# Kernel optimization log

Hardware: AMD Instinct MI355X
Metric: run time of the kernel (lower is better)

The kernel has to match this reference:

```python
import jax, jax.numpy as jnp
import numpy as np
from jax import lax


def ternarize(w):
    """Standard TWN ternarization with straight-through estimator.
    delta = 0.7*mean(|w|); alpha = mean(|w|) over kept entries; w_t = alpha*sign(w)*mask.
    """
    a = jnp.abs(w)
    delta = 0.7 * a.mean()
    mask = (a > delta).astype(w.dtype)
    alpha = (a * mask).sum() / jnp.maximum(mask.sum(), 1.0)
    wt = alpha * jnp.sign(w) * mask
    return w + lax.stop_gradient(wt - w)  # STE


def conv3x3(x, w, b):
    y = lax.conv_general_dilated(x, ternarize(w), window_strides=(1, 1),
                                 padding=((1, 1), (1, 1)),
                                 dimension_numbers=('NCHW', 'OIHW', 'NCHW'))
    return y + b[None, :, None, None]


def maxpool2(x):
    return lax.reduce_window(x, -jnp.inf, lax.max, (1, 1, 2, 2), (1, 1, 2, 2), 'VALID')


def setup_inputs() -> dict:
    key = jax.random.key(0)
    ks = jax.random.split(key, 11)
    s = lambda k, shape, scale: jax.random.normal(k, shape, dtype=jnp.float32) * scale
    return {
        'x':   s(ks[0], (1024, 3, 32, 32), 1.0),
        'w1':  s(ks[1], (64, 3, 3, 3), 0.1),
        'b1':  s(ks[2], (64,), 0.01),
        'w2':  s(ks[3], (128, 64, 3, 3), 0.05),
        'b2':  s(ks[4], (128,), 0.01),
        'w3':  s(ks[5], (256, 128, 3, 3), 0.03),
        'b3':  s(ks[6], (256,), 0.01),
        'wf1': s(ks[7], (256, 4096), 0.02),
        'bf1': s(ks[8], (256,), 0.01),
        'wf2': s(ks[9], (10, 256), 0.06),
        'bf2': s(ks[10], (10,), 0.01),
    }


def reference(x, w1, b1, w2, b2, w3, b3, wf1, bf1, wf2, bf2):
    x = maxpool2(jax.nn.relu(conv3x3(x, w1, b1)))   # [B,64,16,16]
    x = maxpool2(jax.nn.relu(conv3x3(x, w2, b2)))   # [B,128,8,8]
    x = maxpool2(jax.nn.relu(conv3x3(x, w3, b3)))   # [B,256,4,4]
    x = x.reshape(-1, 256 * 4 * 4)
    x = jax.nn.relu(x @ ternarize(wf1).T + bf1)     # [B,256]
    return x @ ternarize(wf2).T + bf2               # [B,10]
```

## Files before the change

### kernel.cpp

```cpp
#include <hip/hip_runtime.h>
#include <hip/hip_bf16.h>


typedef __attribute__((ext_vector_type(8))) short short8;
typedef __attribute__((ext_vector_type(4))) float f32x4;
typedef __attribute__((ext_vector_type(4))) int i32x4;

#define GLOAD_LDS16(g, l)                                              \
    __builtin_amdgcn_global_load_lds(                                  \
        (const __attribute__((address_space(1))) void*)(g),            \
        (__attribute__((address_space(3))) void*)(l), 16, 0, 0)

__device__ __forceinline__ unsigned short f2bf(float x) {
    unsigned u = __float_as_uint(x);
    return (unsigned short)((u + 0x7fffu + ((u >> 16) & 1u)) >> 16);
}
__device__ __forceinline__ float bf2f(unsigned short b) {
    return __uint_as_float(((unsigned)b) << 16);
}

__device__ __forceinline__ float calc_S1(const double* __restrict__ scr,
                                         float amaxx) {
    const double c2 = scr[2];
    const float alpha1 = (float)(scr[1] / (c2 > 1.0 ? c2 : 1.0));
    const float ub = alpha1 * (float)scr[22] * amaxx + (float)scr[23];
    return 32512.0f / fmaxf(ub, 1e-30f);
}
__device__ __forceinline__ float calc_S2(const double* __restrict__ scr,
                                         float amax1) {
    const double c2 = scr[6];
    const float alpha2 = (float)(scr[5] / (c2 > 1.0 ? c2 : 1.0));
    const float ub = alpha2 * (float)scr[24] * amax1 + (float)scr[25];
    return 32512.0f / fmaxf(ub, 1e-30f);
}

#define WS_W1B   0
#define N_W1B    2048
#define WS_W2P   (WS_W1B + N_W1B)
#define N_W2P    (9*128*64)
#define WS_W3P   (WS_W2P + N_W2P)
#define N_W3P    (9*256*128)
#define WS_WTF1  (WS_W3P + N_W3P)
#define N_WTF1   (256*4096)
#define WS_WTF2  (WS_WTF1 + N_WTF1)
#define N_WTF2   (10*256)
#define WS_A1    (WS_WTF2 + N_WTF2)
#define N_A1     (1024*256*64)
#define WS_A2    (WS_A1 + N_A1)
#define N_A2     (1024*64*128)
#define WS_A3    (WS_A2 + N_A2)
#define N_A3     (1024*16*256)
#define WS_F1    (WS_A3 + N_A3)
#define N_F1     (1024*256)
#define WS_SCR   (WS_F1 + N_F1)

#define FC1_S    16

struct TernArgs {
    const float* w[6];
    int n[6];
};

__global__ void tern_stats1(TernArgs ta, double* __restrict__ scr) {
    const int wi = blockIdx.y;
    const float* __restrict__ w = ta.w[wi];
    const int n = ta.n[wi];
    __shared__ double red[4];
    const int lane = threadIdx.x & 63, wv = threadIdx.x >> 6;
    if (wi == 5) {
        float m = 0.f;
        for (int i = blockIdx.x * blockDim.x + threadIdx.x; i < n;
             i += gridDim.x * blockDim.x)
            m = fmaxf(m, fabsf(w[i]));
        #pragma unroll
        for (int off = 32; off > 0; off >>= 1)
            m = fmaxf(m, __shfl_down(m, off, 64));
        if (lane == 0) red[wv] = (double)m;
        __syncthreads();
        if (threadIdx.x == 0) {
            float mm = (float)fmax(fmax(red[0], red[1]), fmax(red[2], red[3]));
            atomicMax((int*)(scr + 20), __float_as_int(mm));
        }
        return;
    }
    double s = 0.0;
    for (int i = blockIdx.x * blockDim.x + threadIdx.x; i < n;
         i += gridDim.x * blockDim.x)
        s += (double)fabsf(w[i]);
    #pragma unroll
    for (int off = 32; off > 0; off >>= 1) s += __shfl_down(s, off, 64);
    if (lane == 0) red[wv] = s;
    __syncthreads();
    if (threadIdx.x == 0)
        atomicAdd(scr + wi * 4, red[0] + red[1] + red[2] + red[3]);
}

__global__ void tern_stats2(TernArgs ta, double* __restrict__ scr) {
    const int wi = blockIdx.y;
    const float* __restrict__ w = ta.w[wi];
    const int n = ta.n[wi];
    const float delta = (float)(0.7 * scr[wi * 4] / (double)n);
    double ms = 0.0, cnt = 0.0;
    for (int i = blockIdx.x * blockDim.x + threadIdx.x; i < n;
         i += gridDim.x * blockDim.x) {
        float a = fabsf(w[i]);
        if (a > delta) { ms += (double)a; cnt += 1.0; }
    }
    #pragma unroll
    for (int off = 32; off > 0; off >>= 1) {
        ms += __shfl_down(ms, off, 64);
        cnt += __shfl_down(cnt, off, 64);
    }
    __shared__ double redm[4], redc[4];
    const int lane = threadIdx.x & 63, wv = threadIdx.x >> 6;
    if (lane == 0) { redm[wv] = ms; redc[wv] = cnt; }
    __syncthreads();
    if (threadIdx.x == 0) {
        atomicAdd(scr + wi * 4 + 1, redm[0] + redm[1] + redm[2] + redm[3]);
        atomicAdd(scr + wi * 4 + 2, redc[0] + redc[1] + redc[2] + redc[3]);
    }
}

__global__ void nnz_pass(const float* __restrict__ w1,
                         const float* __restrict__ b1,
                         const float* __restrict__ w2,
                         const float* __restrict__ b2,
                         double* __restrict__ scr) {
    __shared__ int sc1[2], sc2[2];
    __shared__ float sb1[2], sb2[2];
    const int t = threadIdx.x;
    const int lane = t & 63, wv = t >> 6;

    const float d1 = (float)(0.7 * scr[0] / 1728.0);
    int c1 = 0; float bb1 = 0.f;
    if (t < 64) {
        #pragma unroll
        for (int k = 0; k < 27; k++)
            c1 += (fabsf(w1[t * 27 + k]) > d1) ? 1 : 0;
        bb1 = fabsf(b1[t]);
    }
    const float d2 = (float)(0.7 * scr[4] / 73728.0);
    int c2 = 0;
    for (int k = 0; k < 576; k++)
        c2 += (fabsf(w2[t * 576 + k]) > d2) ? 1 : 0;
    float bb2 = fabsf(b2[t]);

    #pragma unroll
    for (int off = 32; off > 0; off >>= 1) {
        c1 = max(c1, __shfl_down(c1, off, 64));
        c2 = max(c2, __shfl_down(c2, off, 64));
        bb1 = fmaxf(bb1, __shfl_down(bb1, off, 64));
        bb2 = fmaxf(bb2, __shfl_down(bb2, off, 64));
    }
    if (lane == 0) { sc1[wv] = c1; sc2[wv] = c2; sb1[wv] = bb1; sb2[wv] = bb2; }
    __syncthreads();
    if (t == 0) {
        scr[22] = (double)max(sc1[0], sc1[1]);
        scr[23] = (double)fmaxf(sb1[0], sb1[1]);
        scr[24] = (double)max(sc2[0], sc2[1]);
        scr[25] = (double)fmaxf(sb2[0], sb2[1]);
    }
}

__global__ void tern_write_all(TernArgs ta, const double* __restrict__ scr,
                               signed char* __restrict__ w1b,
                               signed char* __restrict__ w2p8,
                               signed char* __restrict__ w3p8,
                               unsigned short* __restrict__ wtf1b,
                               float* __restrict__ wtf2) {
    const int wi = blockIdx.y;
    const float* __restrict__ w = ta.w[wi];
    const int n = ta.n[wi];
    const double* sc = scr + wi * 4;
    const float delta = (float)(0.7 * sc[0] / (double)n);
    const int i0 = blockIdx.x * blockDim.x + threadIdx.x;
    const int stride = gridDim.x * blockDim.x;

    if (wi == 0) {
        for (int i = i0; i < n; i += stride) {
            const int co = i / 27;
            const int kp = i % 27;
            float v = w[i];
            signed char s = (fabsf(v) > delta) ? (v > 0.0f ? 1 : -1) : 0;
            w1b[co * 64 + kp] = s;
            w1b[4096 + co * 64 + 32 + kp] = s;
        }
    } else if (wi == 4) {
        const double c = sc[2];
        const float alpha = (float)(sc[1] / (c > 1.0 ? c : 1.0));
        for (int i = i0; i < n; i += stride) {
            float v = w[i];
            wtf2[i] = (fabsf(v) > delta) ? (v > 0.0f ? alpha : -alpha) : 0.0f;
        }
    } else if (wi == 1 || wi == 2) {
        const int CIc = (wi == 1) ? 64 : 128;
        const int COc = (wi == 1) ? 128 : 256;
        signed char* dst = (wi == 1) ? w2p8 : w3p8;
        for (int i = i0; i < n; i += stride) {
            const int co = i / (CIc * 9);
            const int r = i % (CIc * 9);
            const int ci = r / 9, tap = r % 9;
            float v = w[i];
            signed char s = (fabsf(v) > delta) ? (v > 0.0f ? 1 : -1) : 0;
            dst[(tap * COc + co) * CIc + ci] = s;
        }
    } else {
        for (int i = i0; i < n; i += stride) {
            const int j = i >> 12;
            const int k = i & 4095;
            const int c = k >> 4, px = k & 15;
            float v = w[i];
            unsigned short s = (fabsf(v) > delta) ? (v > 0.0f ? 0x3f80 : 0xbf80) : 0;
            unsigned short* row = wtf1b + ((long)j << 13) + px * 512 + c;
            row[0] = s;
            row[256] = s;
        }
    }
}

__global__ __launch_bounds__(256) void conv1_i8(
        const float* __restrict__ x,
        const signed char* __restrict__ w1b,
        const float* __restrict__ bias,
        const double* __restrict__ scr,
        const int* __restrict__ amax_x,
        int* __restrict__ amax_out,
        signed char* __restrict__ a1q) {
    constexpr int PL = 3472;
    __shared__ __align__(16) char X[2 * PL];
    __shared__ float redm[4];

    const int b = blockIdx.x;
    const int tid = threadIdx.x;
    const float amx = fmaxf(__int_as_float(*amax_x), 1e-30f);
    const float S = 32512.0f / amx;
    const float S1 = calc_S1(scr, __int_as_float(*amax_x));

    for (int i = tid; i < 2 * PL / 16; i += 256)
        ((int4*)X)[i] = make_int4(0, 0, 0, 0);
    __syncthreads();

    for (int i = tid; i < 768; i += 256) {
        const float4 v = ((const float4*)(x + (long)b * 3072))[i];
        const int e = i * 4;
        const int ci = e >> 10;
        const int rem = e & 1023;
        const int h = rem >> 5, w = rem & 31;
        const int base = ci * 1156 + (h + 1) * 34 + (w + 1);
        const float f[4] = {v.x, v.y, v.z, v.w};
        #pragma unroll
        for (int j = 0; j < 4; j++) {
            const int q = __float2int_rn(f[j] * S);
            const int ql = (q << 24) >> 24;
            const int qh = (q - ql) >> 8;
            X[base + j] = (char)ql;
            X[PL + base + j] = (char)qh;
        }
    }
    __syncthreads();

    const int lane = tid & 63;
    const int wid = tid >> 6;
    const int lm = lane & 15;
    const int kg = lane >> 4;

    const int poff = (kg >= 2) ? PL : 0;
    int cst[16];
    #pragma unroll
    for (int j = 0; j < 16; j++) {
        const int kp = (kg & 1) * 16 + j;
        cst[j] = (kp < 27)
                     ? ((kp / 9) * 1156 + ((kp % 9) / 3) * 34 + (kp % 9) % 3)
                     : 0;
    }

    i32x4 BL[4], BH[4];
    #pragma unroll
    for (int nt = 0; nt < 4; nt++) {
        const int co = nt * 16 + lm;
        BL[nt] = *(const i32x4*)(w1b + (long)co * 64 + kg * 16);
        BH[nt] = *(const i32x4*)(w1b + 4096 + (long)co * 64 + kg * 16);
    }

    const double c2 = scr[2];
    const float alpha = (float)(scr[1] / (c2 > 1.0 ? c2 : 1.0));
    const float dq = alpha / S;
    float tmax = 0.f;
    signed char* yb = a1q + (long)b * 32768;

    for (int tt = 0; tt < 16; ++tt) {
        const int t = wid * 16 + tt;
        const int pp = t * 4 + (lm >> 2);
        const int sub = lm & 3;
        const int h = 2 * (pp >> 4) + (sub >> 1);
        const int w = 2 * (pp & 15) + (sub & 1);
        const int base = poff + h * 34 + w;
        unsigned d[4] = {0u, 0u, 0u, 0u};
        #pragma unroll
        for (int j = 0; j < 16; j++) {
            const unsigned byte = (unsigned char)X[base + cst[j]];
            d[j >> 2] |= byte << ((j & 3) * 8);
        }
        i32x4 Af;
        Af[0] = (int)d[0]; Af[1] = (int)d[1];
        Af[2] = (int)d[2]; Af[3] = (int)d[3];

        const int opp = t * 4 + kg;
        const int ho = opp >> 4, wo = opp & 15;
        signed char* yrow = yb + ((long)ho * 2048) + wo * 64;
        #pragma unroll
        for (int nt = 0; nt < 4; nt++) {
            i32x4 aL = 0, aH = 0;
            aL = __builtin_amdgcn_mfma_i32_16x16x64_i8(Af, BL[nt], aL, 0, 0, 0);
            aH = __builtin_amdgcn_mfma_i32_16x16x64_i8(Af, BH[nt], aH, 0, 0, 0);
            const int s0 = aH[0] * 256 + aL[0];
            const int s1 = aH[1] * 256 + aL[1];
            const int s2 = aH[2] * 256 + aL[2];
            const int s3 = aH[3] * 256 + aL[3];
            int sm = s0 > s1 ? s0 : s1;
            const int sn = s2 > s3 ? s2 : s3;
            sm = sm > sn ? sm : sn;
            const int co = nt * 16 + lm;
            const float o = fmaxf(dq * (float)sm + bias[co], 0.f);
            tmax = fmaxf(tmax, o);
            const int q = (int)(o * S1 + 0.5f);
            const int ql = (q << 24) >> 24;
            const int qh = (q + 128) >> 8;
            const int slot = (nt + ((wo + 1) >> 1) + 2 * (ho + 1)) & 3;
            const int off = slot * 16 + lm;
            yrow[off] = (char)ql;
            yrow[1024 + off] = (char)qh;
        }
    }

    #pragma unroll
    for (int off = 32; off > 0; off >>= 1)
        tmax = fmaxf(tmax, __shfl_down(tmax, off, 64));
    if (lane == 0) redm[wid] = tmax;
    __syncthreads();
    if (tid == 0) {
        float m = fmaxf(fmaxf(redm[0], redm[1]), fmaxf(redm[2], redm[3]));
        atomicMax(amax_out, __float_as_int(m));
    }
}

template <int CI, int HI, int CO, int HB, int WM, int WN, int MODE, int WIDX>
__global__ __launch_bounds__(256, 2) void conv_i8(
        const signed char* __restrict__ xin,
        const signed char* __restrict__ wp,
        const float* __restrict__ bias,
        const double* __restrict__ scr,
        const int* __restrict__ amax_x,
        const int* __restrict__ amax_1,
        void* __restrict__ yout) {
    constexpr int CH8 = CI / 64;
    constexpr int NITER = 9 * CH8;
    constexpr int HR = HI / HB;
    constexpr int ROWS = HR + 2;
    constexpr int COLS = HI + 2;
    constexpr int NPIX = ROWS * COLS;
    constexpr int PSTR = NPIX * 64 + 32;
    constexpr int PO = HI / 2;
    constexpr int POR = HR / 2;
    constexpr int MT = 4, NT = 4;
    constexpr int NPL = 2 * CH8;
    constexpr int RWQ = HI * 64 * 2;
    static_assert(WM * WN == 4, "4 waves");
    static_assert(WM * 64 == HR * HI, "M covers slab pixels");
    static_assert(WN * 64 == CO, "N covers all co");
    static_assert(MODE != 0 || (CI == 64 && RWQ == 2048), "conv2 shape");
    static_assert(MODE != 1 || (CI == 128 && HB == 1), "conv3 shape");
    static_assert(HB <= 2, "row compaction assumes <=1 invalid row per end");
    static_assert((COLS & 1) == 0, "swizzle parity uses even COLS");

    __shared__ __align__(16) char X[NPL * PSTR];
    __shared__ __align__(16) char RAW2[(MODE == 1) ? 16384 : 16];

    const int bimg = blockIdx.x / HB;
    const int hb = blockIdx.x % HB;
    const int tid = threadIdx.x;
    const int lane = tid & 63;
    const int wid = tid >> 6;

    const float S_in = (MODE == 0)
                           ? calc_S1(scr, __int_as_float(*amax_x))
                           : calc_S2(scr, __int_as_float(*amax_1));

    const int rlo = (hb == 0) ? 1 : 0;
    const int rhi = (hb == HB - 1) ? (ROWS - 1) : ROWS;

    if (MODE == 0) {
        for (int r = rlo; r < rhi; r++) {
            #pragma unroll
            for (int pl = 0; pl < 2; pl++) {
                if (wid == ((r * 2 + pl) & 3)) {
                    const int h = hb * HR + r - 1;
                    const signed char* src = xin +
                        (long)(bimg * HI + h) * RWQ + pl * 1024 + lane * 16;
                    GLOAD_LDS16(src, &X[pl * PSTR + (r * COLS + 1) * 64]);
                }
            }
        }
    } else {
        #pragma unroll
        for (int j = 0; j < 16; j++) {
            if (wid == (j & 3)) {
                const signed char* src = xin + (long)bimg * 16384 +
                                         j * 1024 + lane * 16;
                GLOAD_LDS16(src, &RAW2[j * 1024]);
            }
        }
    }

    {
        const int nfull = ((hb == 0) ? 1 : 0) + ((hb == HB - 1) ? 1 : 0);
        const int NP1 = ROWS * 2;
        const int NPZ = NP1 + nfull * (COLS - 2);
        for (int i = tid; i < NPZ * NPL * 4; i += 256) {
            const int u = i & 3;
            const int t = i >> 2;
            const int g = t % NPL;
            const int e = t / NPL;
            int p;
            if (e < NP1) {
                const int row = e >> 1;
                p = row * COLS + ((e & 1) ? (COLS - 1) : 0);
            } else {
                const int e2 = e - NP1;
                const int inFirst = (hb == 0) && (e2 < COLS - 2);
                const int fr = inFirst ? 0 : (ROWS - 1);
                const int cc = inFirst ? e2
                                       : (e2 - ((hb == 0) ? (COLS - 2) : 0));
                p = fr * COLS + 1 + cc;
            }
            *(int4*)&X[g * PSTR + p * 64 + u * 16] = make_int4(0, 0, 0, 0);
        }
    }

    if (MODE == 1) {
        __syncthreads();
        #pragma unroll
        for (int k = 0; k < 16; k++) {
            const int v = tid + k * 256;
            const int h = v >> 9;
            const int r = v & 511;
            const int g = r >> 7;
            const int b4 = (r & 127) << 2;
            const unsigned d = *(const unsigned*)&RAW2[v << 2];
            *(unsigned*)&X[g * PSTR + ((h + 1) * COLS + 1) * 64 + b4] = d;
        }
    }
    __syncthreads();

    const int wm = (WM == 1) ? 0 : (wid >> 1);
    const int wn = (WM == 1) ? wid : (wid & 1);
    const int lm = lane & 15;
    const int kg = lane >> 4;

    int pq[MT];
    #pragma unroll
    for (int mt = 0; mt < MT; mt++) {
        const int m = (wm * MT + mt) * 16 + lm;
        const int pp = m >> 2, sub = m & 3;
        const int lph = pp / PO, lpw = pp % PO;
        const int h = 2 * lph + (sub >> 1);
        const int w = 2 * lpw + (sub & 1);
        pq[mt] = ((h * COLS + w) << 6) | ((h & 1) << 3) | (w & 7);
    }
    const signed char* bp[NT];
    #pragma unroll
    for (int nt = 0; nt < NT; nt++) {
        const int co = (wn * NT + nt) * 16 + lm;
        bp[nt] = wp + (long)co * CI + kg * 16;
    }

    i32x4 accL[MT][NT], accH[MT][NT];
    #pragma unroll
    for (int mt = 0; mt < MT; mt++)
        #pragma unroll
        for (int nt = 0; nt < NT; nt++) { accL[mt][nt] = 0; accH[mt][nt] = 0; }

    i32x4 Bb[2][NT];
    #pragma unroll
    for (int nt = 0; nt < NT; nt++) Bb[0][nt] = *(const i32x4*)(bp[nt]);

    #pragma unroll 2
    for (int it = 0; it < NITER; ++it) {
        const int cur = it & 1, nxt = cur ^ 1;
        if (it + 1 < NITER) {
            const int it1 = it + 1;
            const int tap = it1 / CH8, ch1 = it1 % CH8;
            const int woff = tap * CO * CI + ch1 * 64;
            #pragma unroll
            for (int nt = 0; nt < NT; nt++)
                Bb[nxt][nt] = *(const i32x4*)(bp[nt] + woff);
        }
        const int tap = it / CH8, ch = it % CH8;
        const int ty = tap / 3, tx = tap % 3;
        const int DT = (ty * COLS + tx) << 6;
        const int typ = ty & 1;
        int ao[MT];
        #pragma unroll
        for (int mt = 0; mt < MT; mt++) {
            const int q = pq[mt];
            const int slot = (kg + ((((q >> 3) & 1) + typ) & 1) * 2 +
                              (((q & 7) + tx) >> 1)) & 3;
            ao[mt] = (q & ~63) + DT + (slot << 4);
        }
        {
            i32x4 Af[MT];
            #pragma unroll
            for (int mt = 0; mt < MT; mt++)
                Af[mt] = *(const i32x4*)&X[ch * PSTR + ao[mt]];
            #pragma unroll
            for (int mt = 0; mt < MT; mt++)
                #pragma unroll
                for (int nt = 0; nt < NT; nt++)
                    accL[mt][nt] = __builtin_amdgcn_mfma_i32_16x16x64_i8(
                        Af[mt], Bb[cur][nt], accL[mt][nt], 0, 0, 0);
        }
        {
            i32x4 Af[MT];
            #pragma unroll
            for (int mt = 0; mt < MT; mt++)
                Af[mt] = *(const i32x4*)&X[(CH8 + ch) * PSTR + ao[mt]];
            #pragma unroll
            for (int mt = 0; mt < MT; mt++)
                #pragma unroll
                for (int nt = 0; nt < NT; nt++)
                    accH[mt][nt] = __builtin_amdgcn_mfma_i32_16x16x64_i8(
                        Af[mt], Bb[cur][nt], accH[mt][nt], 0, 0, 0);
        }
    }

    const double* wst = scr + WIDX * 4;
    const double c2 = wst[2];
    const float alpha = (float)(wst[1] / (c2 > 1.0 ? c2 : 1.0));
    const float dq = alpha / S_in;
    if (MODE == 0) {
        const float S2 = calc_S2(scr, __int_as_float(*amax_1));
        signed char* oq = (signed char*)yout;
        #pragma unroll
        for (int mt = 0; mt < MT; mt++) {
            const int pp = (wm * MT + mt) * 4 + kg;
            const int lph = pp / PO, lpw = pp % PO;
            const int h = hb * POR + lph;
            const int w = lpw;
            #pragma unroll
            for (int nt = 0; nt < NT; nt++) {
                const int co2 = (wn * NT + nt) * 16 + lm;
                const i32x4 aL = accL[mt][nt], aH = accH[mt][nt];
                int s0 = aH[0] * 256 + aL[0];
                int s1 = aH[1] * 256 + aL[1];
                int s2 = aH[2] * 256 + aL[2];
                int s3 = aH[3] * 256 + aL[3];
                int sm = s0 > s1 ? s0 : s1;
                int sn = s2 > s3 ? s2 : s3;
                sm = sm > sn ? sm : sn;
                const float o = fmaxf(dq * (float)sm + bias[co2], 0.f);
                const int q = (int)(o * S2 + 0.5f);
                const int ql = (q << 24) >> 24;
                const int qh = (q + 128) >> 8;
                const int slot = (((co2 >> 4) & 3) + ((w + 1) >> 1) +
                                  2 * (h + 1)) & 3;
                const long base = (long)bimg * 16384 + h * 2048 +
                                  (co2 >> 6) * 512 + w * 64 + slot * 16 +
                                  (co2 & 15);
                oq[base] = (char)ql;
                oq[base + 1024] = (char)qh;
            }
        }
    } else {
        unsigned short* yo = (unsigned short*)yout;
        #pragma unroll
        for (int mt = 0; mt < MT; mt++) {
            const int pp = (wm * MT + mt) * 4 + kg;
            const int lph = pp / PO, lpw = pp % PO;
            const int gpp = (hb * POR + lph) * PO + lpw;
            unsigned short* yr = yo + ((long)bimg * (PO * PO) + gpp) * (2 * CO);
            #pragma unroll
            for (int nt = 0; nt < NT; nt++) {
                const int co = (wn * NT + nt) * 16 + lm;
                const i32x4 aL = accL[mt][nt], aH = accH[mt][nt];
                int s0 = aH[0] * 256 + aL[0];
                int s1 = aH[1] * 256 + aL[1];
                int s2 = aH[2] * 256 + aL[2];
                int s3 = aH[3] * 256 + aL[3];
                int sm = s0 > s1 ? s0 : s1;
                int sn = s2 > s3 ? s2 : s3;
                sm = sm > sn ? sm : sn;
                float o = fmaxf(dq * (float)sm + bias[co], 0.f);
                unsigned short hi = f2bf(o);
                unsigned short lo = f2bf(o - bf2f(hi));
                yr[co] = hi;
                yr[CO + co] = lo;
            }
        }
    }
}

template <int S>
__global__ __launch_bounds__(256) void fc1_mfma(
        const unsigned short* __restrict__ A,
        const unsigned short* __restrict__ Bw,
        float* __restrict__ parts) {
    constexpr int KCH = 8192 / S;
    constexpr int NSTEP = KCH / 32;
    const int m0 = blockIdx.x * 128;
    const int n0 = blockIdx.y * 128;
    const int s = blockIdx.z;
    const int tid = threadIdx.x;
    const int lane = tid & 63, wid = tid >> 6;
    const int wm = wid >> 1, wn = wid & 1;
    const int lm = lane & 15, kg = lane >> 4;

    const long k0 = (long)s * KCH + kg * 8;
    const unsigned short* ap[4];
    const unsigned short* bp[4];
    #pragma unroll
    for (int t = 0; t < 4; t++) {
        ap[t] = A + (long)(m0 + wm * 64 + t * 16 + lm) * 8192 + k0;
        bp[t] = Bw + (long)(n0 + wn * 64 + t * 16 + lm) * 8192 + k0;
    }

    f32x4 acc[4][4] = {};
    short8 Ab[2][4], Bb[2][4];
    #pragma unroll
    for (int t = 0; t < 4; t++) {
        Ab[0][t] = *(const short8*)(ap[t]);
        Bb[0][t] = *(const short8*)(bp[t]);
    }

    #pragma unroll 2
    for (int st = 0; st < NSTEP; ++st) {
        const int cur = st & 1, nxt = cur ^ 1;
        if (st + 1 < NSTEP) {
            const int off = (st + 1) * 32;
            #pragma unroll
            for (int t = 0; t < 4; t++) {
                Ab[nxt][t] = *(const short8*)(ap[t] + off);
                Bb[nxt][t] = *(const short8*)(bp[t] + off);
            }
        }
        #pragma unroll
        for (int mt = 0; mt < 4; mt++)
            #pragma unroll
            for (int nt = 0; nt < 4; nt++)
                acc[mt][nt] = __builtin_amdgcn_mfma_f32_16x16x32_bf16(
                    Ab[cur][mt], Bb[cur][nt], acc[mt][nt], 0, 0, 0);
    }

    #pragma unroll
    for (int mt = 0; mt < 4; mt++) {
        #pragma unroll
        for (int r = 0; r < 4; r++) {
            const int b = m0 + wm * 64 + mt * 16 + kg * 4 + r;
            #pragma unroll
            for (int nt = 0; nt < 4; nt++) {
                const int j = n0 + wn * 64 + nt * 16 + lm;
                parts[((long)s * 1024 + b) * 256 + j] = acc[mt][nt][r];
            }
        }
    }
}

template <int S>
__global__ __launch_bounds__(256) void fc2_fused(
        const float* __restrict__ parts,
        const double* __restrict__ scr,
        const float* __restrict__ bf1v,
        const float* __restrict__ wtf2,
        const float* __restrict__ bf2v,
        float* __restrict__ out) {
    __shared__ float sf[256];
    const int b = blockIdx.x;
    const int j = threadIdx.x;
    float s = 0.f;
    #pragma unroll
    for (int p = 0; p < S; p++)
        s += parts[(long)p * 262144 + (long)b * 256 + j];
    const double c2 = scr[2];
    const float alpha = (float)(scr[1] / (c2 > 1.0 ? c2 : 1.0));
    sf[j] = fmaxf(alpha * s + bf1v[j], 0.f);
    __syncthreads();
    const int lane = threadIdx.x & 63, wid = threadIdx.x >> 6;
    for (int k = wid; k < 10; k += 4) {
        const float* wr = wtf2 + k * 256;
        float acc = 0.f;
        #pragma unroll
        for (int t = 0; t < 4; t++)
            acc += sf[lane + t * 64] * wr[lane + t * 64];
        #pragma unroll
        for (int off = 32; off > 0; off >>= 1)
            acc += __shfl_down(acc, off, 64);
        if (lane == 0) out[(long)b * 10 + k] = acc + bf2v[k];
    }
}

extern "C" void kernel_launch(void* const* d_in, const int* in_sizes, int n_in,
                              void* d_out, int out_size, void* d_ws, size_t ws_size,
                              hipStream_t stream) {
    const float* x   = (const float*)d_in[0];
    const float* w1  = (const float*)d_in[1];
    const float* b1  = (const float*)d_in[2];
    const float* w2  = (const float*)d_in[3];
    const float* b2  = (const float*)d_in[4];
    const float* w3  = (const float*)d_in[5];
    const float* b3  = (const float*)d_in[6];
    const float* wf1 = (const float*)d_in[7];
    const float* bf1 = (const float*)d_in[8];
    const float* wf2 = (const float*)d_in[9];
    const float* bf2 = (const float*)d_in[10];
    float* out = (float*)d_out;
    float* ws = (float*)d_ws;

    const int B = 1024;

    signed char*    w1b   = (signed char*)(ws + WS_W1B);
    signed char*    w2p8  = (signed char*)(ws + WS_W2P);
    signed char*    w3p8  = (signed char*)(ws + WS_W3P);
    unsigned short* wtf1b = (unsigned short*)(ws + WS_WTF1);
    float*          wtf2  = ws + WS_WTF2;
    signed char*    a1q   = (signed char*)(ws + WS_A1);
    signed char*    a2q   = (signed char*)(ws + WS_A2);
    unsigned short* a3p   = (unsigned short*)(ws + WS_A3);
    double*         scr   = (double*)(ws + WS_SCR);
    int*            iscr  = (int*)(scr + 20);
    int*            amaxx = iscr;
    int*            amax1 = iscr + 1;
    float*          parts = ws + WS_A1;

    hipMemsetAsync(scr, 0, 26 * sizeof(double), stream);
    hipMemsetAsync(w1b, 0, 8192, stream);

    TernArgs ta;
    ta.w[0] = w1;  ta.n[0] = 64 * 27;
    ta.w[1] = w2;  ta.n[1] = 128 * 64 * 9;
    ta.w[2] = w3;  ta.n[2] = 256 * 128 * 9;
    ta.w[3] = wf1; ta.n[3] = 256 * 4096;
    ta.w[4] = wf2; ta.n[4] = 10 * 256;
    ta.w[5] = x;   ta.n[5] = 1024 * 3 * 32 * 32;

    hipLaunchKernelGGL(tern_stats1, dim3(128, 6), dim3(256), 0, stream, ta, scr);
    hipLaunchKernelGGL(tern_stats2, dim3(128, 5), dim3(256), 0, stream, ta, scr);
    hipLaunchKernelGGL(nnz_pass, dim3(1), dim3(128), 0, stream,
                       w1, b1, w2, b2, scr);
    hipLaunchKernelGGL(tern_write_all, dim3(128, 5), dim3(256), 0, stream,
                       ta, scr, w1b, w2p8, w3p8, wtf1b, wtf2);

    hipLaunchKernelGGL(conv1_i8, dim3(B), dim3(256), 0, stream,
                       x, w1b, b1, scr, amaxx, amax1, a1q);

    hipLaunchKernelGGL((conv_i8<64, 16, 128, 2, 2, 2, 0, 1>), dim3(B * 2),
                       dim3(256), 0, stream, a1q, w2p8, b2, scr, amaxx,
                       amax1, a2q);

    hipLaunchKernelGGL((conv_i8<128, 8, 256, 1, 1, 4, 1, 2>), dim3(B),
                       dim3(256), 0, stream, a2q, w3p8, b3, scr, amaxx,
                       amax1, a3p);

    hipLaunchKernelGGL((fc1_mfma<FC1_S>), dim3(8, 2, FC1_S), dim3(256), 0, stream,
                       a3p, wtf1b, parts);

    hipLaunchKernelGGL((fc2_fused<FC1_S>), dim3(B), dim3(256), 0, stream,
                       parts, scr + 12, bf1, wtf2, bf2, out);
}
```

Before: 284.8 us.

## Quantize conv3 output to int8 hi/lo and run fc1 with int8 MFMA

Conv3 now writes its ReLU output as an int8 hi/lo pair scaled by a new S3 factor instead of a bf16 hi/lo pair. The scale comes from the running max of conv2 outputs, tracked with an atomic. The fc1 GEMM switches from bf16 MFMA to i32 16x16x64 int8 MFMA using int8 ternary weights, with twice as many K splits. The nnz/bias-max statistics move out of the single-block nnz_pass kernel into an extra slice of tern_stats2, which also covers conv3. Together these halve the bytes moved for the activations and fc1 weights and remove one launch. The cost is a block-wide reduction plus a __syncthreads in conv2, more partial sums for fc2 to add up, and a bound-based quantization whose accuracy depends on the statistics.

```diff
diff --git a/kernel.cpp b/kernel.cpp
--- a/kernel.cpp
+++ b/kernel.cpp
@@ -21,16 +21,26 @@
 
 __device__ __forceinline__ float calc_S1(const double* __restrict__ scr,
                                          float amaxx) {
+    const int* ii = (const int*)(scr + 20);
     const double c2 = scr[2];
     const float alpha1 = (float)(scr[1] / (c2 > 1.0 ? c2 : 1.0));
-    const float ub = alpha1 * (float)scr[22] * amaxx + (float)scr[23];
+    const float ub = alpha1 * (float)ii[3] * amaxx + __int_as_float(ii[6]);
     return 32512.0f / fmaxf(ub, 1e-30f);
 }
 __device__ __forceinline__ float calc_S2(const double* __restrict__ scr,
                                          float amax1) {
+    const int* ii = (const int*)(scr + 20);
     const double c2 = scr[6];
     const float alpha2 = (float)(scr[5] / (c2 > 1.0 ? c2 : 1.0));
-    const float ub = alpha2 * (float)scr[24] * amax1 + (float)scr[25];
+    const float ub = alpha2 * (float)ii[4] * amax1 + __int_as_float(ii[7]);
+    return 32512.0f / fmaxf(ub, 1e-30f);
+}
+__device__ __forceinline__ float calc_S3(const double* __restrict__ scr,
+                                         float amax2) {
+    const int* ii = (const int*)(scr + 20);
+    const double c2 = scr[10];
+    const float alpha3 = (float)(scr[9] / (c2 > 1.0 ? c2 : 1.0));
+    const float ub = alpha3 * (float)ii[5] * amax2 + __int_as_float(ii[8]);
     return 32512.0f / fmaxf(ub, 1e-30f);
 }
 
@@ -54,7 +64,7 @@
 #define N_F1     (1024*256)
 #define WS_SCR   (WS_F1 + N_F1)
 
-#define FC1_S    16
+#define FC1_S    32
 
 struct TernArgs {
     const float* w[6];
@@ -95,8 +105,59 @@
         atomicAdd(scr + wi * 4, red[0] + red[1] + red[2] + red[3]);
 }
 
-__global__ void tern_stats2(TernArgs ta, double* __restrict__ scr) {
+__global__ void tern_stats2(TernArgs ta,
+                            const float* __restrict__ b1v,
+                            const float* __restrict__ b2v,
+                            const float* __restrict__ b3v,
+                            double* __restrict__ scr) {
     const int wi = blockIdx.y;
+    const int lane = threadIdx.x & 63, wv = threadIdx.x >> 6;
+
+    if (wi == 5) {
+        int* ii = (int*)(scr + 20);
+        const int gw = blockIdx.x * 4 + wv;
+        if (gw < 64) {
+            const float d = (float)(0.7 * scr[0] / 1728.0);
+            const float* row = ta.w[0] + gw * 27;
+            int c = (lane < 27) ? (fabsf(row[lane]) > d ? 1 : 0) : 0;
+            #pragma unroll
+            for (int off = 32; off > 0; off >>= 1)
+                c += __shfl_down(c, off, 64);
+            if (lane == 0) atomicMax(ii + 3, c);
+        } else if (gw < 192) {
+            const float d = (float)(0.7 * scr[4] / 73728.0);
+            const float* row = ta.w[1] + (long)(gw - 64) * 576;
+            int c = 0;
+            for (int k = lane; k < 576; k += 64)
+                c += (fabsf(row[k]) > d) ? 1 : 0;
+            #pragma unroll
+            for (int off = 32; off > 0; off >>= 1)
+                c += __shfl_down(c, off, 64);
+            if (lane == 0) atomicMax(ii + 4, c);
+        } else if (gw < 448) {
+            const float d = (float)(0.7 * scr[8] / 294912.0);
+            const float* row = ta.w[2] + (long)(gw - 192) * 1152;
+            int c = 0;
+            for (int k = lane; k < 1152; k += 64)
+                c += (fabsf(row[k]) > d) ? 1 : 0;
+            #pragma unroll
+            for (int off = 32; off > 0; off >>= 1)
+                c += __shfl_down(c, off, 64);
+            if (lane == 0) atomicMax(ii + 5, c);
+        } else if (gw < 451) {
+            const float* bv = (gw == 448) ? b1v : (gw == 449) ? b2v : b3v;
+            const int nb = (gw == 448) ? 64 : (gw == 449) ? 128 : 256;
+            float m = 0.f;
+            for (int k = lane; k < nb; k += 64) m = fmaxf(m, fabsf(bv[k]));
+            #pragma unroll
+            for (int off = 32; off > 0; off >>= 1)
+                m = fmaxf(m, __shfl_down(m, off, 64));
+            if (lane == 0)
+                atomicMax(ii + 6 + (gw - 448), __float_as_int(m));
+        }
+        return;
+    }
+
     const float* __restrict__ w = ta.w[wi];
     const int n = ta.n[wi];
     const float delta = (float)(0.7 * scr[wi * 4] / (double)n);
@@ -112,7 +173,6 @@
         cnt += __shfl_down(cnt, off, 64);
     }
     __shared__ double redm[4], redc[4];
-    const int lane = threadIdx.x & 63, wv = threadIdx.x >> 6;
     if (lane == 0) { redm[wv] = ms; redc[wv] = cnt; }
     __syncthreads();
     if (threadIdx.x == 0) {
@@ -121,52 +181,11 @@
     }
 }
 
-__global__ void nnz_pass(const float* __restrict__ w1,
-                         const float* __restrict__ b1,
-                         const float* __restrict__ w2,
-                         const float* __restrict__ b2,
-                         double* __restrict__ scr) {
-    __shared__ int sc1[2], sc2[2];
-    __shared__ float sb1[2], sb2[2];
-    const int t = threadIdx.x;
-    const int lane = t & 63, wv = t >> 6;
-
-    const float d1 = (float)(0.7 * scr[0] / 1728.0);
-    int c1 = 0; float bb1 = 0.f;
-    if (t < 64) {
-        #pragma unroll
-        for (int k = 0; k < 27; k++)
-            c1 += (fabsf(w1[t * 27 + k]) > d1) ? 1 : 0;
-        bb1 = fabsf(b1[t]);
-    }
-    const float d2 = (float)(0.7 * scr[4] / 73728.0);
-    int c2 = 0;
-    for (int k = 0; k < 576; k++)
-        c2 += (fabsf(w2[t * 576 + k]) > d2) ? 1 : 0;
-    float bb2 = fabsf(b2[t]);
-
-    #pragma unroll
-    for (int off = 32; off > 0; off >>= 1) {
-        c1 = max(c1, __shfl_down(c1, off, 64));
-        c2 = max(c2, __shfl_down(c2, off, 64));
-        bb1 = fmaxf(bb1, __shfl_down(bb1, off, 64));
-        bb2 = fmaxf(bb2, __shfl_down(bb2, off, 64));
-    }
-    if (lane == 0) { sc1[wv] = c1; sc2[wv] = c2; sb1[wv] = bb1; sb2[wv] = bb2; }
-    __syncthreads();
-    if (t == 0) {
-        scr[22] = (double)max(sc1[0], sc1[1]);
-        scr[23] = (double)fmaxf(sb1[0], sb1[1]);
-        scr[24] = (double)max(sc2[0], sc2[1]);
-        scr[25] = (double)fmaxf(sb2[0], sb2[1]);
-    }
-}
-
 __global__ void tern_write_all(TernArgs ta, const double* __restrict__ scr,
                                signed char* __restrict__ w1b,
                                signed char* __restrict__ w2p8,
                                signed char* __restrict__ w3p8,
-                               unsigned short* __restrict__ wtf1b,
+                               signed char* __restrict__ wtf1b8,
                                float* __restrict__ wtf2) {
     const int wi = blockIdx.y;
     const float* __restrict__ w = ta.w[wi];
@@ -208,12 +227,10 @@
         for (int i = i0; i < n; i += stride) {
             const int j = i >> 12;
             const int k = i & 4095;
-            const int c = k >> 4, px = k & 15;
+            const int px = k & 15, c = k >> 4;
             float v = w[i];
-            unsigned short s = (fabsf(v) > delta) ? (v > 0.0f ? 0x3f80 : 0xbf80) : 0;
-            unsigned short* row = wtf1b + ((long)j << 13) + px * 512 + c;
-            row[0] = s;
-            row[256] = s;
+            signed char s = (fabsf(v) > delta) ? (v > 0.0f ? 1 : -1) : 0;
+            wtf1b8[(long)j * 4096 + px * 256 + c] = s;
         }
     }
 }
@@ -352,6 +369,7 @@
         const double* __restrict__ scr,
         const int* __restrict__ amax_x,
         const int* __restrict__ amax_1,
+        int* __restrict__ amax_2,
         void* __restrict__ yout) {
     constexpr int CH8 = CI / 64;
     constexpr int NITER = 9 * CH8;
@@ -375,6 +393,7 @@
 
     __shared__ __align__(16) char X[NPL * PSTR];
     __shared__ __align__(16) char RAW2[(MODE == 1) ? 16384 : 16];
+    __shared__ float redm[4];
 
     const int bimg = blockIdx.x / HB;
     const int hb = blockIdx.x % HB;
@@ -540,6 +559,7 @@
     if (MODE == 0) {
         const float S2 = calc_S2(scr, __int_as_float(*amax_1));
         signed char* oq = (signed char*)yout;
+        float tmax = 0.f;
         #pragma unroll
         for (int mt = 0; mt < MT; mt++) {
             const int pp = (wm * MT + mt) * 4 + kg;
@@ -558,6 +578,7 @@
                 int sn = s2 > s3 ? s2 : s3;
                 sm = sm > sn ? sm : sn;
                 const float o = fmaxf(dq * (float)sm + bias[co2], 0.f);
+                tmax = fmaxf(tmax, o);
                 const int q = (int)(o * S2 + 0.5f);
                 const int ql = (q << 24) >> 24;
                 const int qh = (q + 128) >> 8;
@@ -570,14 +591,24 @@
                 oq[base + 1024] = (char)qh;
             }
         }
+        #pragma unroll
+        for (int off = 32; off > 0; off >>= 1)
+            tmax = fmaxf(tmax, __shfl_down(tmax, off, 64));
+        if (lane == 0) redm[wid] = tmax;
+        __syncthreads();
+        if (tid == 0) {
+            float m = fmaxf(fmaxf(redm[0], redm[1]), fmaxf(redm[2], redm[3]));
+            atomicMax(amax_2, __float_as_int(m));
+        }
     } else {
-        unsigned short* yo = (unsigned short*)yout;
+        const float S3 = calc_S3(scr, __int_as_float(*amax_2));
+        signed char* oq = (signed char*)yout;
         #pragma unroll
         for (int mt = 0; mt < MT; mt++) {
             const int pp = (wm * MT + mt) * 4 + kg;
             const int lph = pp / PO, lpw = pp % PO;
             const int gpp = (hb * POR + lph) * PO + lpw;
-            unsigned short* yr = yo + ((long)bimg * (PO * PO) + gpp) * (2 * CO);
+            signed char* yr = oq + (long)bimg * 8192 + gpp * 512;
             #pragma unroll
             for (int nt = 0; nt < NT; nt++) {
                 const int co = (wn * NT + nt) * 16 + lm;
@@ -589,23 +620,24 @@
                 int sm = s0 > s1 ? s0 : s1;
                 int sn = s2 > s3 ? s2 : s3;
                 sm = sm > sn ? sm : sn;
-                float o = fmaxf(dq * (float)sm + bias[co], 0.f);
-                unsigned short hi = f2bf(o);
-                unsigned short lo = f2bf(o - bf2f(hi));
-                yr[co] = hi;
-                yr[CO + co] = lo;
+                const float o = fmaxf(dq * (float)sm + bias[co], 0.f);
+                const int q = (int)(o * S3 + 0.5f);
+                const int ql = (q << 24) >> 24;
+                const int qh = (q + 128) >> 8;
+                yr[co] = (char)ql;
+                yr[256 + co] = (char)qh;
             }
         }
     }
 }
 
 template <int S>
-__global__ __launch_bounds__(256) void fc1_mfma(
-        const unsigned short* __restrict__ A,
-        const unsigned short* __restrict__ Bw,
+__global__ __launch_bounds__(256) void fc1_i8(
+        const signed char* __restrict__ A,
+        const signed char* __restrict__ Bw,
         float* __restrict__ parts) {
-    constexpr int KCH = 8192 / S;
-    constexpr int NSTEP = KCH / 32;
+    constexpr int KCH = 4096 / S;
+    constexpr int NCH = KCH / 64;
     const int m0 = blockIdx.x * 128;
     const int n0 = blockIdx.y * 128;
     const int s = blockIdx.z;
@@ -614,40 +646,41 @@
     const int wm = wid >> 1, wn = wid & 1;
     const int lm = lane & 15, kg = lane >> 4;
 
-    const long k0 = (long)s * KCH + kg * 8;
-    const unsigned short* ap[4];
-    const unsigned short* bp[4];
+    const int k0 = s * KCH;
+    const signed char* ap[4];
+    const signed char* bp[4];
     #pragma unroll
     for (int t = 0; t < 4; t++) {
-        ap[t] = A + (long)(m0 + wm * 64 + t * 16 + lm) * 8192 + k0;
-        bp[t] = Bw + (long)(n0 + wn * 64 + t * 16 + lm) * 8192 + k0;
-    }
-
-    f32x4 acc[4][4] = {};
-    short8 Ab[2][4], Bb[2][4];
-    #pragma unroll
-    for (int t = 0; t < 4; t++) {
-        Ab[0][t] = *(const short8*)(ap[t]);
-        Bb[0][t] = *(const short8*)(bp[t]);
-    }
-
-    #pragma unroll 2
-    for (int st = 0; st < NSTEP; ++st) {
-        const int cur = st & 1, nxt = cur ^ 1;
-        if (st + 1 < NSTEP) {
-            const int off = (st + 1) * 32;
-            #pragma unroll
-            for (int t = 0; t < 4; t++) {
-                Ab[nxt][t] = *(const short8*)(ap[t] + off);
-                Bb[nxt][t] = *(const short8*)(bp[t] + off);
+        ap[t] = A + (long)(m0 + wm * 64 + t * 16 + lm) * 8192;
+        bp[t] = Bw + (long)(n0 + wn * 64 + t * 16 + lm) * 4096 + k0 + kg * 16;
+    }
+
+    i32x4 accL[4][4], accH[4][4];
+    #pragma unroll
+    for (int mt = 0; mt < 4; mt++)
+        #pragma unroll
+        for (int nt = 0; nt < 4; nt++) { accL[mt][nt] = 0; accH[mt][nt] = 0; }
+
+    #pragma unroll
+    for (int ch = 0; ch < NCH; ++ch) {
+        const int kb = k0 + ch * 64;
+        const int aoff = (kb >> 8) * 512 + (kb & 255) + kg * 16;
+        i32x4 Ah[4], Al[4], Bb[4];
+        #pragma unroll
+        for (int t = 0; t < 4; t++) {
+            Al[t] = *(const i32x4*)(ap[t] + aoff);
+            Ah[t] = *(const i32x4*)(ap[t] + aoff + 256);
+            Bb[t] = *(const i32x4*)(bp[t] + ch * 64);
+        }
+        #pragma unroll
+        for (int mt = 0; mt < 4; mt++)
+            #pragma unroll
+            for (int nt = 0; nt < 4; nt++) {
+                accH[mt][nt] = __builtin_amdgcn_mfma_i32_16x16x64_i8(
+                    Ah[mt], Bb[nt], accH[mt][nt], 0, 0, 0);
+                accL[mt][nt] = __builtin_amdgcn_mfma_i32_16x16x64_i8(
+                    Al[mt], Bb[nt], accL[mt][nt], 0, 0, 0);
             }
-        }
-        #pragma unroll
-        for (int mt = 0; mt < 4; mt++)
-            #pragma unroll
-            for (int nt = 0; nt < 4; nt++)
-                acc[mt][nt] = __builtin_amdgcn_mfma_f32_16x16x32_bf16(
-                    Ab[cur][mt], Bb[cur][nt], acc[mt][nt], 0, 0, 0);
     }
 
     #pragma unroll
@@ -658,7 +691,8 @@
             #pragma unroll
             for (int nt = 0; nt < 4; nt++) {
                 const int j = n0 + wn * 64 + nt * 16 + lm;
-                parts[((long)s * 1024 + b) * 256 + j] = acc[mt][nt][r];
+                const int sum = accH[mt][nt][r] * 256 + accL[mt][nt][r];
+                parts[((long)s * 1024 + b) * 256 + j] = (float)sum;
             }
         }
     }
@@ -668,6 +702,7 @@
 __global__ __launch_bounds__(256) void fc2_fused(
         const float* __restrict__ parts,
         const double* __restrict__ scr,
+        const int* __restrict__ amax_2,
         const float* __restrict__ bf1v,
         const float* __restrict__ wtf2,
         const float* __restrict__ bf2v,
@@ -679,9 +714,10 @@
     #pragma unroll
     for (int p = 0; p < S; p++)
         s += parts[(long)p * 262144 + (long)b * 256 + j];
-    const double c2 = scr[2];
-    const float alpha = (float)(scr[1] / (c2 > 1.0 ? c2 : 1.0));
-    sf[j] = fmaxf(alpha * s + bf1v[j], 0.f);
+    const double c2 = scr[14];
+    const float alpha = (float)(scr[13] / (c2 > 1.0 ? c2 : 1.0));
+    const float S3 = calc_S3(scr, __int_as_float(*amax_2));
+    sf[j] = fmaxf(alpha * s / S3 + bf1v[j], 0.f);
     __syncthreads();
     const int lane = threadIdx.x & 63, wid = threadIdx.x >> 6;
     for (int k = wid; k < 10; k += 4) {
@@ -719,15 +755,16 @@
     signed char*    w1b   = (signed char*)(ws + WS_W1B);
     signed char*    w2p8  = (signed char*)(ws + WS_W2P);
     signed char*    w3p8  = (signed char*)(ws + WS_W3P);
-    unsigned short* wtf1b = (unsigned short*)(ws + WS_WTF1);
+    signed char*    wtf1b8 = (signed char*)(ws + WS_WTF1);
     float*          wtf2  = ws + WS_WTF2;
     signed char*    a1q   = (signed char*)(ws + WS_A1);
     signed char*    a2q   = (signed char*)(ws + WS_A2);
-    unsigned short* a3p   = (unsigned short*)(ws + WS_A3);
+    signed char*    a3q   = (signed char*)(ws + WS_A3);
     double*         scr   = (double*)(ws + WS_SCR);
     int*            iscr  = (int*)(scr + 20);
     int*            amaxx = iscr;
     int*            amax1 = iscr + 1;
+    int*            amax2 = iscr + 2;
     float*          parts = ws + WS_A1;
 
     hipMemsetAsync(scr, 0, 26 * sizeof(double), stream);
@@ -742,26 +779,25 @@
     ta.w[5] = x;   ta.n[5] = 1024 * 3 * 32 * 32;
 
     hipLaunchKernelGGL(tern_stats1, dim3(128, 6), dim3(256), 0, stream, ta, scr);
-    hipLaunchKernelGGL(tern_stats2, dim3(128, 5), dim3(256), 0, stream, ta, scr);
-    hipLaunchKernelGGL(nnz_pass, dim3(1), dim3(128), 0, stream,
-                       w1, b1, w2, b2, scr);
+    hipLaunchKernelGGL(tern_stats2, dim3(128, 6), dim3(256), 0, stream,
+                       ta, b1, b2, b3, scr);
     hipLaunchKernelGGL(tern_write_all, dim3(128, 5), dim3(256), 0, stream,
-                       ta, scr, w1b, w2p8, w3p8, wtf1b, wtf2);
+                       ta, scr, w1b, w2p8, w3p8, wtf1b8, wtf2);
 
     hipLaunchKernelGGL(conv1_i8, dim3(B), dim3(256), 0, stream,
                        x, w1b, b1, scr, amaxx, amax1, a1q);
 
     hipLaunchKernelGGL((conv_i8<64, 16, 128, 2, 2, 2, 0, 1>), dim3(B * 2),
                        dim3(256), 0, stream, a1q, w2p8, b2, scr, amaxx,
-                       amax1, a2q);
+                       amax1, amax2, a2q);
 
     hipLaunchKernelGGL((conv_i8<128, 8, 256, 1, 1, 4, 1, 2>), dim3(B),
                        dim3(256), 0, stream, a2q, w3p8, b3, scr, amaxx,
-                       amax1, a3p);
-
-    hipLaunchKernelGGL((fc1_mfma<FC1_S>), dim3(8, 2, FC1_S), dim3(256), 0, stream,
-                       a3p, wtf1b, parts);
+                       amax1, amax2, a3q);
+
+    hipLaunchKernelGGL((fc1_i8<FC1_S>), dim3(8, 2, FC1_S), dim3(256), 0, stream,
+                       a3q, wtf1b8, parts);
 
     hipLaunchKernelGGL((fc2_fused<FC1_S>), dim3(B), dim3(256), 0, stream,
-                       parts, scr + 12, bf1, wtf2, bf2, out);
-}
+                       parts, scr, amax2, bf1, wtf2, bf2, out);
+}
```

Measured after the change: 269.5 us. 1.06x faster.
